# Optimization experiments

Measured on AMD Instinct MI355X. Metric: run time of the kernel, lower is better.

The kernel has to match this reference:

```python
import jax, jax.numpy as jnp
import numpy as np

L, B, S, D, N, H = 4, 4, 1024, 1024, 64, 16   # layers, batch, seq, d_model, d_state, heads
DI = 2 * D      # d_inner (expand_factor=2)
DH = D // H     # head dim
DF = 4 * D      # ffn hidden
SCALE = 1.0 / np.sqrt(DH)


def setup_inputs() -> dict:
    key = jax.random.key(0)
    ks = jax.random.split(key, 12)
    w = lambda k, sh: jax.random.normal(k, sh, jnp.float32) * 0.02
    return {
        "x": jax.random.normal(ks[0], (B, S, D), jnp.float32),
        "A_log": jax.random.normal(ks[1], (L, N), jnp.float32),
        "Dp": jax.random.normal(ks[2], (L, D), jnp.float32),
        "W_in": w(ks[3], (L, 2 * DI, D)), "b_in": jnp.zeros((L, 2 * DI), jnp.float32),
        "W_xp": w(ks[4], (L, N, DI)), "b_xp": jnp.zeros((L, N), jnp.float32),
        "W_dt": w(ks[5], (L, D, DI)), "b_dt": jnp.zeros((L, D), jnp.float32),
        "W_out": w(ks[6], (L, D, DI)), "b_out": jnp.zeros((L, D), jnp.float32),
        "W_qkv": w(ks[7], (L, 3 * D, D)), "b_qkv": jnp.zeros((L, 3 * D), jnp.float32),
        "W_ao": w(ks[8], (L, D, D)), "b_ao": jnp.zeros((L, D), jnp.float32),
        "g1": jnp.ones((L, D), jnp.float32), "be1": jnp.zeros((L, D), jnp.float32),
        "g2": jnp.ones((L, D), jnp.float32), "be2": jnp.zeros((L, D), jnp.float32),
        "W_f1": w(ks[9], (L, DF, D)), "b_f1": jnp.zeros((L, DF), jnp.float32),
        "W_f2": w(ks[10], (L, D, DF)), "b_f2": jnp.zeros((L, D), jnp.float32),
    }


def _ln(x, g, b, eps=1e-5):
    mu = x.mean(-1, keepdims=True)
    var = ((x - mu) ** 2).mean(-1, keepdims=True)
    return (x - mu) * jax.lax.rsqrt(var + eps) * g + b


def _mamba(x, A_log, Dp, W_in, b_in, W_xp, b_xp, W_dt, b_dt, W_out, b_out):
    xr = jnp.einsum('bsd,od->bso', x, W_in) + b_in          # [b,s,2*DI]
    xi, res = jnp.split(xr, 2, axis=-1)
    xi = jax.nn.silu(xi)
    A = -jnp.exp(A_log)                                      # [N]
    delta = jax.nn.softplus(jnp.einsum('bsi,di->bsd', xi, W_dt) + b_dt)  # [b,s,D]
    m = delta.mean(-1)                                       # [b,s]
    A_disc = jnp.exp(A[None, None, :] * m[:, :, None])       # [b,s,N]
    u = jnp.einsum('bsi,ni->bsn', xi, W_xp) + b_xp           # [b,s,N]

    def step(state, inp):
        a_t, u_t = inp
        state = a_t * state + u_t                            # [b,N]
        return state, state.sum(-1)                          # carry, emit sum over d_state

    init = jnp.zeros((x.shape[0], A_log.shape[0]), x.dtype)
    _, ssum = jax.lax.scan(step, init, (A_disc.swapaxes(0, 1), u.swapaxes(0, 1)))
    ssum = ssum.swapaxes(0, 1)                               # [b,s]
    y = ssum[..., None] * xi                                 # [b,s,DI]
    y = y * jax.nn.silu(res)
    y = jnp.einsum('bsi,di->bsd', y, W_out) + b_out
    return y + x * Dp


def _attn(x, W_qkv, b_qkv, W_ao, b_ao):
    b, s, d = x.shape
    qkv = jnp.einsum('bsd,od->bso', x, W_qkv) + b_qkv        # [b,s,3d]
    qkv = qkv.reshape(b, s, 3, H, DH)
    q = jnp.moveaxis(qkv[:, :, 0], 2, 1)                     # [b,h,s,dh]
    k = jnp.moveaxis(qkv[:, :, 1], 2, 1)
    v = jnp.moveaxis(qkv[:, :, 2], 2, 1)
    scores = jnp.einsum('bhqd,bhkd->bhqk', q, k) * SCALE
    wts = jax.nn.softmax(scores, axis=-1)
    o = jnp.einsum('bhqk,bhkd->bhqd', wts, v)
    o = jnp.moveaxis(o, 1, 2).reshape(b, s, d)
    return jnp.einsum('bsd,od->bso', o, W_ao) + b_ao


def _forward(x, A_log, Dp, W_in, b_in, W_xp, b_xp, W_dt, b_dt, W_out, b_out,
             W_qkv, b_qkv, W_ao, b_ao, g1, be1, g2, be2, W_f1, b_f1, W_f2, b_f2):
    for l in range(L):
        m = _mamba(x, A_log[l], Dp[l], W_in[l], b_in[l], W_xp[l], b_xp[l],
                   W_dt[l], b_dt[l], W_out[l], b_out[l])
        x = _ln(x + m, g1[l], be1[l])
        a = _attn(x, W_qkv[l], b_qkv[l], W_ao[l], b_ao[l])
        x = _ln(x + a, g2[l], be2[l])
        h = jax.nn.gelu(jnp.einsum('bsd,fd->bsf', x, W_f1[l]) + b_f1[l], approximate=False)
        x = x + jnp.einsum('bsf,df->bsd', h, W_f2[l]) + b_f2[l]
    return x


def reference(x, A_log, Dp, W_in, b_in, W_xp, b_xp, W_dt, b_dt, W_out, b_out,
              W_qkv, b_qkv, W_ao, b_ao, g1, be1, g2, be2, W_f1, b_f1, W_f2, b_f2):
    return _forward(x, A_log, Dp, W_in, b_in, W_xp, b_xp, W_dt, b_dt, W_out, b_out,
                    W_qkv, b_qkv, W_ao, b_ao, g1, be1, g2, be2, W_f1, b_f1, W_f2, b_f2)
```

## Files before the change

kernel.cpp:

```cpp
#include <hip/hip_runtime.h>
#include <math.h>

typedef unsigned short ushort_t;
typedef unsigned int uint_t;
typedef __attribute__((ext_vector_type(8))) short short8;
typedef __attribute__((ext_vector_type(4))) float f32x4;

constexpr int Bb = 4, Ss = 1024, Dd = 1024, Nn = 64, Hh = 16;
constexpr int DIi = 2048, DFf = 4096;
constexpr int TOKENS = Bb * Ss;

constexpr size_t O_IN  = 0;
constexpr size_t O_DT  = 4194304;
constexpr size_t O_XP  = O_DT + 2097152;
constexpr size_t O_OUT = O_XP + 262144;
constexpr size_t O_QKV = O_OUT + 2097152;
constexpr size_t O_AO  = O_QKV + 3145728;
constexpr size_t O_F1  = O_AO + 1048576;
constexpr size_t O_F2  = O_F1 + 4194304;
constexpr size_t W_TOTAL = O_F2 + 4194304;
constexpr size_t W_QUADS = W_TOTAL / 4;

enum { EPI_SPLIT = 0, EPI_QKV, EPI_GELU, EPI_DTXP, EPI_DP, EPI_F32, EPI_RESID };

__device__ __forceinline__ float siluf(float x) { return x / (1.f + expf(-x)); }
__device__ __forceinline__ float softplusf(float x) { return fmaxf(x, 0.f) + log1pf(expf(-fabsf(x))); }
__device__ __forceinline__ float geluf(float x) { return 0.5f * x * (1.f + erff(x * 0.7071067811865476f)); }

__device__ __forceinline__ float bf2f(uint_t u) {
    union { uint_t i; float f; } v; v.i = u << 16; return v.f;
}
__device__ __forceinline__ ushort_t f2bf(float f) {
    union { float f; uint_t i; } v; v.f = f;
    return (ushort_t)((v.i + 0x7FFFu + ((v.i >> 16) & 1u)) >> 16);
}

__device__ __forceinline__ void gload_lds16(const ushort_t* g, ushort_t* l) {
    __builtin_amdgcn_global_load_lds(
        (const __attribute__((address_space(1))) unsigned int*)g,
        (__attribute__((address_space(3))) unsigned int*)l, 16, 0, 0);
}

__device__ __forceinline__ void wait_vm(int n) {
    if (n == 0)      asm volatile("s_waitcnt vmcnt(0)" ::: "memory");
    else if (n == 3) asm volatile("s_waitcnt vmcnt(3)" ::: "memory");
    else if (n == 4) asm volatile("s_waitcnt vmcnt(4)" ::: "memory");
    else if (n == 6) asm volatile("s_waitcnt vmcnt(6)" ::: "memory");
    else             asm volatile("s_waitcnt vmcnt(8)" ::: "memory");
}

template <int EPI>
__global__ __launch_bounds__(512, 2) void gemm_wide256(
    const ushort_t* __restrict__ A, const ushort_t* __restrict__ Bw,
    const float* __restrict__ bias, int M, int N, int K,
    ushort_t* __restrict__ ob0, ushort_t* __restrict__ ob1)
{
    __shared__ __attribute__((aligned(16))) ushort_t AB[65536];
    const int tid = threadIdx.x;
    const int lane = tid & 63, wid = tid >> 6;
    const int wr = wid >> 2, wc = wid & 3;
    const int l15 = lane & 15, lg = lane >> 4;

    int bx = blockIdx.x, by = blockIdx.y;
    const int gx = gridDim.x, gy = gridDim.y;
    if ((gy & 3) == 0 && (gx & 1) == 0) {
        const int s = by * gx + bx;
        const int xcd = s & 7, c = s >> 3;
        const int gyc = gy >> 2, gxc = gx >> 1;
        by = (xcd & 3) * gyc + (c % gyc);
        bx = (xcd >> 2) * gxc + (c / gyc);
    }
    const int m0 = by << 8, n0 = bx << 8;

    f32x4 acc[8][4];
#pragma unroll
    for (int i = 0; i < 8; ++i)
#pragma unroll
        for (int j = 0; j < 4; ++j) { acc[i][j][0]=0.f; acc[i][j][1]=0.f; acc[i][j][2]=0.f; acc[i][j][3]=0.f; }

    const int srow8 = lane >> 3;
    const int scc8  = (lane & 7) ^ srow8;
    const ushort_t* Ag = A + (size_t)(m0 + wid * 32 + srow8) * K + scc8 * 8;
    const ushort_t* Bg = Bw + (size_t)(n0 + wid * 32 + srow8) * K + scc8 * 8;

    auto STAGE = [&](int b_, int k0_) {
        ushort_t* d_ = AB + b_ * 32768;
#pragma unroll
        for (int i = 0; i < 4; ++i) {
            gload_lds16(Ag + (size_t)i * 8 * K + k0_, d_ + (wid * 32 + i * 8) * 64);
            gload_lds16(Bg + (size_t)i * 8 * K + k0_, d_ + 16384 + (wid * 32 + i * 8) * 64);
        }
    };

    const int NS = K >> 6;
    STAGE(0, 0);
    wait_vm(0);
    __builtin_amdgcn_s_barrier();
    int cur = 0;
    for (int s = 0; s < NS; ++s) {
        if (s + 1 < NS) STAGE(cur ^ 1, (s + 1) << 6);
        const ushort_t* As_ = AB + cur * 32768;
        const ushort_t* Bs_ = As_ + 16384;
#pragma unroll
        for (int kk = 0; kk < 2; ++kk) {
            short8 af[8], bfr[4];
#pragma unroll
            for (int mi = 0; mi < 8; ++mi) {
                const int row = wr * 128 + mi * 16 + l15;
                const int ch = (kk * 4 + lg) ^ (row & 7);
                af[mi] = *(const short8*)&As_[row * 64 + ch * 8];
            }
#pragma unroll
            for (int nj = 0; nj < 4; ++nj) {
                const int row = wc * 64 + nj * 16 + l15;
                const int ch = (kk * 4 + lg) ^ (row & 7);
                bfr[nj] = *(const short8*)&Bs_[row * 64 + ch * 8];
            }
#pragma unroll
            for (int mi = 0; mi < 8; ++mi)
#pragma unroll
                for (int nj = 0; nj < 4; ++nj)
                    acc[mi][nj] = __builtin_amdgcn_mfma_f32_16x16x32_bf16(
                        af[mi], bfr[nj], acc[mi][nj], 0, 0, 0);
        }
        if (s + 1 < NS) {
            wait_vm(0);
            __builtin_amdgcn_s_barrier();
        }
        cur ^= 1;
    }
    __syncthreads();

    const bool lo = (EPI != EPI_SPLIT) || (n0 < DIi);
#pragma unroll
    for (int nj = 0; nj < 4; ++nj) {
        const int coll = wc * 64 + nj * 16 + l15;
        const float bv = bias[n0 + coll];
#pragma unroll
        for (int mi = 0; mi < 8; ++mi)
#pragma unroll
            for (int r = 0; r < 4; ++r) {
                float v = acc[mi][nj][r] + bv;
                if (EPI == EPI_SPLIT) v = lo ? siluf(v) : v;
                else v = geluf(v);
                AB[(wr * 128 + mi * 16 + lg * 4 + r) * 256 + coll] = f2bf(v);
            }
    }
    __syncthreads();
    ushort_t* dst = (EPI == EPI_SPLIT) ? (lo ? ob0 : ob1) : ob0;
    const int Nd = (EPI == EPI_SPLIT) ? DIi : N;
    const int nb = (EPI == EPI_SPLIT && !lo) ? (n0 - DIi) : n0;
#pragma unroll
    for (int it = 0; it < 16; ++it) {
        const int c = it * 512 + tid;
        const int row = c >> 5, ch = c & 31;
        *(uint4*)&dst[(size_t)(m0 + row) * Nd + nb + ch * 8] =
            *(const uint4*)&AB[row * 256 + ch * 8];
    }
}

template <int EPI, int MT, int NBUF, int XBY>
__global__ __launch_bounds__(256) void gemm_mfma(
    const ushort_t* __restrict__ A, const ushort_t* __restrict__ Bw,
    const float* __restrict__ bias, int M, int N, int K,
    float* __restrict__ of0, float* __restrict__ of1,
    ushort_t* __restrict__ ob0, ushort_t* __restrict__ ob1,
    const float* __restrict__ e0, const float* __restrict__ e1)
{
    constexpr int BUFSZ = (MT == 128) ? 8192 : 6144;
    constexpr int DEPTH = NBUF - 1;
    constexpr int L     = (MT == 128) ? 4 : 3;
    constexpr int NJ    = (MT == 128) ? 4 : 2;
    constexpr int XBX   = 8 / XBY;
    __shared__ __attribute__((aligned(16))) ushort_t AB[NBUF * BUFSZ];

    const int tid = threadIdx.x;
    const int lane = tid & 63, wid = tid >> 6;
    const int wr = (MT == 128) ? (wid >> 1) : 0;
    const int wc = (MT == 128) ? (wid & 1) : wid;
    const int l15 = lane & 15, lg = lane >> 4;

    int bx = blockIdx.x, by = blockIdx.y;
    const int gx = gridDim.x, gy = gridDim.y;
    if ((gy % XBY) == 0 && (gx % XBX) == 0) {
        const int s = by * gx + bx;
        const int xcd = s & 7, c = s >> 3;
        const int gyc = gy / XBY, gxc = gx / XBX;
        by = (xcd % XBY) * gyc + (c % gyc);
        bx = (xcd / XBY) * gxc + (c / gyc);
    }
    const int m0 = by * MT, n0 = bx << 7;

    f32x4 acc[4][NJ];
#pragma unroll
    for (int i = 0; i < 4; ++i)
#pragma unroll
        for (int j = 0; j < NJ; ++j) { acc[i][j][0] = 0.f; acc[i][j][1] = 0.f; acc[i][j][2] = 0.f; acc[i][j][3] = 0.f; }

    const int srow4 = lane >> 2;
    const int scc4  = (lane & 3) ^ ((lane >> 3) & 3);
    const ushort_t* Ag = A + (size_t)(m0 + wid * 32 + srow4) * K + scc4 * 8;
    const ushort_t* Bg = Bw + (size_t)(n0 + wid * 32 + srow4) * K + scc4 * 8;
    const ushort_t* sb64[3];
    int do64[3];
    if (MT == 64) {
#pragma unroll
        for (int j = 0; j < 3; ++j) {
            const int i = wid * 3 + j;
            const bool isA = i < 4;
            const int rb = (isA ? i : i - 4) * 16;
            sb64[j] = (isA ? A + (size_t)(m0 + rb + srow4) * K
                           : Bw + (size_t)(n0 + rb + srow4) * K) + scc4 * 8;
            do64[j] = (isA ? 0 : 2048) + rb * 32;
        }
    }

    auto STAGE = [&](int b_, int k0_) {
        ushort_t* d_ = AB + b_ * BUFSZ;
        if constexpr (MT == 128) {
            gload_lds16(Ag + k0_,                  d_ + (wid * 32) * 32);
            gload_lds16(Ag + (size_t)16 * K + k0_, d_ + (wid * 32 + 16) * 32);
            gload_lds16(Bg + k0_,                  d_ + 4096 + (wid * 32) * 32);
            gload_lds16(Bg + (size_t)16 * K + k0_, d_ + 4096 + (wid * 32 + 16) * 32);
        } else {
#pragma unroll
            for (int j = 0; j < 3; ++j)
                gload_lds16(sb64[j] + k0_, d_ + do64[j]);
        }
    };

    const int NS = K >> 5;
#pragma unroll
    for (int p = 0; p < DEPTH; ++p) STAGE(p, p * 32);
    wait_vm((DEPTH - 1) * L);
    __builtin_amdgcn_s_barrier();

    const int chAB = (lg ^ ((l15 >> 1) & 3)) * 8;
    int bc = 0, bp = DEPTH;
    for (int s = 0; s < NS; ++s) {
        if (s + DEPTH < NS) STAGE(bp, (s + DEPTH) << 5);
        const ushort_t* As_ = AB + bc * BUFSZ;
        const ushort_t* Bs_ = As_ + ((MT == 128) ? 4096 : 2048);
        short8 af[4], bfr[NJ];
#pragma unroll
        for (int mi = 0; mi < 4; ++mi)
            af[mi] = *(const short8*)&As_[(wr * 64 + mi * 16 + l15) * 32 + chAB];
#pragma unroll
        for (int nj = 0; nj < NJ; ++nj)
            bfr[nj] = *(const short8*)&Bs_[(wc * (MT == 128 ? 64 : 32) + nj * 16 + l15) * 32 + chAB];
#pragma unroll
        for (int mi = 0; mi < 4; ++mi)
#pragma unroll
            for (int nj = 0; nj < NJ; ++nj)
                acc[mi][nj] = __builtin_amdgcn_mfma_f32_16x16x32_bf16(
                    af[mi], bfr[nj], acc[mi][nj], 0, 0, 0);
        if (s + 1 < NS) {
            const int rem = NS - 2 - s;
            wait_vm(((rem < DEPTH - 1) ? rem : DEPTH - 1) * L);
            __builtin_amdgcn_s_barrier();
        }
        bc = (bc + 1 == NBUF) ? 0 : bc + 1;
        bp = (bp + 1 == NBUF) ? 0 : bp + 1;
    }
    __syncthreads();

    if constexpr (MT == 128) {
        const bool lo = (EPI != EPI_SPLIT) || (n0 < DIi);
#pragma unroll
        for (int nj = 0; nj < 4; ++nj) {
            const int coll = wc * 64 + nj * 16 + l15;
            const float bv = bias[n0 + coll];
#pragma unroll
            for (int mi = 0; mi < 4; ++mi)
#pragma unroll
                for (int r = 0; r < 4; ++r) {
                    float v = acc[mi][nj][r] + bv;
                    if (EPI == EPI_SPLIT) v = lo ? siluf(v) : v;
                    else if (EPI == EPI_GELU) v = geluf(v);
                    AB[(wr * 64 + mi * 16 + lg * 4 + r) * 128 + coll] = f2bf(v);
                }
        }
        __syncthreads();
        if (EPI == EPI_QKV && n0 >= 2048) {
            const int bb = m0 >> 10, srow0 = m0 & 1023;
#pragma unroll
            for (int it = 0; it < 8; ++it) {
                const int task = it * 256 + tid;
                const int dim = task & 127;
                const int strip = task >> 7;
                uint_t w[4];
#pragma unroll
                for (int j = 0; j < 4; ++j) {
                    const int s2 = strip * 8 + 2 * j;
                    w[j] = (uint_t)AB[s2 * 128 + dim] | ((uint_t)AB[(s2 + 1) * 128 + dim] << 16);
                }
                const int vd = (n0 - 2048) + dim;
                *(uint4*)&ob1[((size_t)(bb * Hh + (vd >> 6)) * 64 + (vd & 63)) * Ss + srow0 + strip * 8] =
                    make_uint4(w[0], w[1], w[2], w[3]);
            }
        } else {
            ushort_t* dst = (EPI == EPI_SPLIT) ? (lo ? ob0 : ob1) : ob0;
            const int Nd = (EPI == EPI_SPLIT) ? DIi : N;
            const int nb = (EPI == EPI_SPLIT && !lo) ? (n0 - DIi) : n0;
#pragma unroll
            for (int i = 0; i < 8; ++i) {
                const int c = i * 256 + tid;
                const int row = c >> 4, ch = c & 15;
                *(uint4*)&dst[(size_t)(m0 + row) * Nd + nb + ch * 8] =
                    *(const uint4*)&AB[row * 128 + ch * 8];
            }
        }
    } else {
        float* Cf = (float*)AB;
#pragma unroll
        for (int nj = 0; nj < NJ; ++nj) {
            const int coll = wc * 32 + nj * 16 + l15;
            const float bv = bias[n0 + coll];
#pragma unroll
            for (int mi = 0; mi < 4; ++mi)
#pragma unroll
                for (int r = 0; r < 4; ++r)
                    Cf[(mi * 16 + lg * 4 + r) * 128 + coll] = acc[mi][nj][r] + bv;
        }
        __syncthreads();
#pragma unroll
        for (int i = 0; i < 8; ++i) {
            const int c = i * 256 + tid;
            const int row = c >> 5, ch = c & 31;
            const int grow = m0 + row;
            const int gcol = n0 + ch * 4;
            float4 v = *(const float4*)&Cf[row * 128 + ch * 4];
            if (EPI == EPI_DTXP) {
                if (n0 < Dd) {
                    float ps = softplusf(v.x) + softplusf(v.y) + softplusf(v.z) + softplusf(v.w);
#pragma unroll
                    for (int off = 1; off < 32; off <<= 1) ps += __shfl_xor(ps, off);
                    if ((lane & 31) == 0)
                        of0[(size_t)grow * 8 + (n0 >> 7)] = ps;
                } else {
                    *(float4*)&of1[(size_t)grow * 128 + (gcol - Dd)] = v;
                }
            } else if (EPI == EPI_DP) {
                const float4 e = *(const float4*)&e0[(size_t)grow * N + gcol];
                const float4 d = *(const float4*)&e1[gcol];
                v.x = fmaf(e.x, d.x, v.x); v.y = fmaf(e.y, d.y, v.y);
                v.z = fmaf(e.z, d.z, v.z); v.w = fmaf(e.w, d.w, v.w);
                *(float4*)&of0[(size_t)grow * N + gcol] = v;
            } else if (EPI == EPI_F32) {
                *(float4*)&of0[(size_t)grow * N + gcol] = v;
            } else {
                const float4 e = *(const float4*)&e0[(size_t)grow * N + gcol];
                v.x += e.x; v.y += e.y; v.z += e.z; v.w += e.w;
                *(float4*)&of0[(size_t)grow * N + gcol] = v;
                uint2 w;
                w.x = (uint_t)f2bf(v.x) | ((uint_t)f2bf(v.y) << 16);
                w.y = (uint_t)f2bf(v.z) | ((uint_t)f2bf(v.w) << 16);
                *(uint2*)&ob0[(size_t)grow * N + gcol] = w;
            }
        }
    }
}

__global__ __launch_bounds__(256) void convert_weights_kernel(
    const float* __restrict__ Win, const float* __restrict__ Wdt,
    const float* __restrict__ Wxp, const float* __restrict__ Wout,
    const float* __restrict__ Wqkv, const float* __restrict__ Wao,
    const float* __restrict__ Wf1, const float* __restrict__ Wf2,
    const float* __restrict__ bdt, const float* __restrict__ bxp,
    ushort_t* __restrict__ dst, float* __restrict__ bcat)
{
    size_t q = (size_t)blockIdx.x * blockDim.x + threadIdx.x;
    if (q < 288) {
#pragma unroll
        for (int j = 0; j < 4; ++j) {
            const int e = (int)q * 4 + j;
            bcat[e] = (e < Dd) ? bdt[e] : ((e < Dd + Nn) ? bxp[e - Dd] : 0.f);
        }
    }
    const size_t stride = (size_t)gridDim.x * blockDim.x;
    for (; q < W_QUADS; q += stride) {
        const size_t e = q * 4;
        float4 v;
        if (e < O_DT)       v = *(const float4*)&Win[e - O_IN];
        else if (e < O_XP)  v = *(const float4*)&Wdt[e - O_DT];
        else if (e < O_OUT) {
            const size_t li = e - O_XP;
            const int row = (int)(li >> 11), colq = (int)(li & 2047);
            v = (row < Nn) ? *(const float4*)&Wxp[(size_t)row * DIi + colq]
                           : make_float4(0.f, 0.f, 0.f, 0.f);
        }
        else if (e < O_QKV) v = *(const float4*)&Wout[e - O_OUT];
        else if (e < O_AO)  v = *(const float4*)&Wqkv[e - O_QKV];
        else if (e < O_F1)  v = *(const float4*)&Wao[e - O_AO];
        else if (e < O_F2)  v = *(const float4*)&Wf1[e - O_F1];
        else                v = *(const float4*)&Wf2[e - O_F2];
        uint2 w;
        w.x = (uint_t)f2bf(v.x) | ((uint_t)f2bf(v.y) << 16);
        w.y = (uint_t)f2bf(v.z) | ((uint_t)f2bf(v.w) << 16);
        *(uint2*)&dst[e] = w;
    }
}

__global__ __launch_bounds__(256) void cvt_f32_bf16_kernel(
    const float* __restrict__ in, ushort_t* __restrict__ out)
{
    const size_t i4 = (size_t)blockIdx.x * blockDim.x + threadIdx.x;
    const float4 v = *(const float4*)&in[i4 * 4];
    uint2 w;
    w.x = (uint_t)f2bf(v.x) | ((uint_t)f2bf(v.y) << 16);
    w.y = (uint_t)f2bf(v.z) | ((uint_t)f2bf(v.w) << 16);
    *(uint2*)&out[i4 * 4] = w;
}

__global__ __launch_bounds__(256) void ln_residual_kernel(
    float* __restrict__ xio, const float* __restrict__ addin,
    const float* __restrict__ g, const float* __restrict__ be,
    ushort_t* __restrict__ xb)
{
    __shared__ float red[8];
    const int tid = threadIdx.x;
    const size_t base = (size_t)blockIdx.x * Dd;
    const float4 xv = *(const float4*)&xio[base + tid * 4];
    const float4 av = *(const float4*)&addin[base + tid * 4];
    float v[4] = {xv.x + av.x, xv.y + av.y, xv.z + av.z, xv.w + av.w};
    float s = v[0] + v[1] + v[2] + v[3];
    float s2 = v[0] * v[0] + v[1] * v[1] + v[2] * v[2] + v[3] * v[3];
#pragma unroll
    for (int off = 32; off; off >>= 1) { s += __shfl_xor(s, off); s2 += __shfl_xor(s2, off); }
    if ((tid & 63) == 0) { red[tid >> 6] = s; red[4 + (tid >> 6)] = s2; }
    __syncthreads();
    const float mu = (red[0] + red[1] + red[2] + red[3]) * (1.f / (float)Dd);
    const float var = (red[4] + red[5] + red[6] + red[7]) * (1.f / (float)Dd) - mu * mu;
    const float rstd = rsqrtf(var + 1e-5f);
    const float4 gv = *(const float4*)&g[tid * 4];
    const float4 bv = *(const float4*)&be[tid * 4];
    float o[4];
    o[0] = (v[0] - mu) * rstd * gv.x + bv.x;
    o[1] = (v[1] - mu) * rstd * gv.y + bv.y;
    o[2] = (v[2] - mu) * rstd * gv.z + bv.z;
    o[3] = (v[3] - mu) * rstd * gv.w + bv.w;
    *(float4*)&xio[base + tid * 4] = make_float4(o[0], o[1], o[2], o[3]);
    uint2 w;
    w.x = (uint_t)f2bf(o[0]) | ((uint_t)f2bf(o[1]) << 16);
    w.y = (uint_t)f2bf(o[2]) | ((uint_t)f2bf(o[3]) << 16);
    *(uint2*)&xb[base + tid * 4] = w;
}

__global__ __launch_bounds__(1024) void scan_fused_kernel(
    const float* __restrict__ A_log_l, const float* __restrict__ part,
    const float* __restrict__ u, float* __restrict__ ssum)
{
    __shared__ float Ps[16][64];
    __shared__ float Sl[16][64];
    __shared__ float Cs[16][64];
    __shared__ float Ms[16][64];
    const int b = blockIdx.x;
    const int tid = threadIdx.x;
    const int n = tid & 63, c = tid >> 6;
    const int t0 = b * Ss + c * 64;
    const float Aval = -expf(A_log_l[n]);

    {
        const float* pp = part + (size_t)(t0 + n) * 8;
        float ps = 0.f;
#pragma unroll
        for (int j = 0; j < 8; ++j) ps += pp[j];
        Ms[c][n] = ps * (1.f / 1024.f);
    }
    __syncthreads();

    float S = 0.f, msum = 0.f;
#pragma unroll 8
    for (int t = 0; t < 64; ++t) {
        const float mt = Ms[c][t];
        msum += mt;
        S = fmaf(expf(Aval * mt), S, u[(size_t)(t0 + t) * 128 + n]);
    }
    Ps[c][n] = expf(Aval * msum);
    Sl[c][n] = S;
    __syncthreads();

    if (c == 0) {
        float carry = 0.f;
#pragma unroll
        for (int cc = 0; cc < 16; ++cc) {
            Cs[cc][n] = carry;
            carry = fmaf(Ps[cc][n], carry, Sl[cc][n]);
        }
    }
    __syncthreads();

    float st = Cs[c][n];
#pragma unroll 4
    for (int t = 0; t < 64; ++t) {
        st = fmaf(expf(Aval * Ms[c][t]), st, u[(size_t)(t0 + t) * 128 + n]);
        float r = st;
#pragma unroll
        for (int off = 32; off; off >>= 1) r += __shfl_xor(r, off);
        if (n == 0) ssum[t0 + t] = r;
    }
}

__global__ __launch_bounds__(256) void y_gate_kernel(
    ushort_t* __restrict__ xi, const ushort_t* __restrict__ res,
    const float* __restrict__ ssum)
{
    const size_t i8 = (size_t)blockIdx.x * blockDim.x + threadIdx.x;
    const int t = (int)(i8 >> 8);
    const float sv = ssum[t];
    uint4 xw = *(const uint4*)&xi[i8 * 8];
    const uint4 rw = *(const uint4*)&res[i8 * 8];
    const uint_t xs[4] = {xw.x, xw.y, xw.z, xw.w};
    const uint_t rs[4] = {rw.x, rw.y, rw.z, rw.w};
    uint_t os[4];
#pragma unroll
    for (int j = 0; j < 4; ++j) {
        const float x0 = bf2f(xs[j] & 0xffffu), x1 = bf2f(xs[j] >> 16);
        const float r0 = bf2f(rs[j] & 0xffffu), r1 = bf2f(rs[j] >> 16);
        os[j] = (uint_t)f2bf(sv * x0 * siluf(r0)) | ((uint_t)f2bf(sv * x1 * siluf(r1)) << 16);
    }
    *(uint4*)&xi[i8 * 8] = make_uint4(os[0], os[1], os[2], os[3]);
}

__global__ __launch_bounds__(256) void attn_mfma_kernel(
    const ushort_t* __restrict__ qkv, const ushort_t* __restrict__ vt,
    ushort_t* __restrict__ out)
{
    __shared__ ushort_t Ks[2][64 * 64];
    __shared__ ushort_t Vs[2][64 * 64];
    __shared__ __attribute__((aligned(16))) ushort_t Pb[4][2560];

    const int tid = threadIdx.x;
    const int lane = tid & 63, wid = tid >> 6;
    const int b = blockIdx.z, h = blockIdx.y;
    const int q0 = blockIdx.x * 128 + wid * 32;
    const int l15 = lane & 15, lg = lane >> 4;
    constexpr float CEXP = 0.125f * 1.44269504f;

    short8 qf[2][2];
#pragma unroll
    for (int mi = 0; mi < 2; ++mi)
#pragma unroll
        for (int kk = 0; kk < 2; ++kk)
            qf[mi][kk] = *(const short8*)&qkv[(size_t)(b * Ss + q0 + mi * 16 + l15) * 3072
                                              + h * 64 + kk * 32 + lg * 8];

    f32x4 oacc[2][4];
#pragma unroll
    for (int mi = 0; mi < 2; ++mi)
#pragma unroll
        for (int nj = 0; nj < 4; ++nj) { oacc[mi][nj][0]=0.f; oacc[mi][nj][1]=0.f; oacc[mi][nj][2]=0.f; oacc[mi][nj][3]=0.f; }
    float lrun[2][4];
#pragma unroll
    for (int mi = 0; mi < 2; ++mi)
#pragma unroll
        for (int r = 0; r < 4; ++r) lrun[mi][r] = 0.f;

    const int srow = lane >> 3;
    const int scc  = (lane & 7) ^ srow;
    const ushort_t* Kg = qkv + (size_t)(b * Ss + wid * 16 + srow) * 3072 + 1024 + h * 64 + scc * 8;
    const ushort_t* Vg = vt + (size_t)((b * Hh + h) * 64 + wid * 16 + srow) * Ss + scc * 8;

    auto STAGE_KV = [&](int buf, int kt) {
#pragma unroll
        for (int j = 0; j < 2; ++j) {
            gload_lds16(Kg + (size_t)(kt * 64 + j * 8) * 3072, Ks[buf] + (wid * 16 + j * 8) * 64);
            gload_lds16(Vg + (size_t)j * 8 * Ss + kt * 64,     Vs[buf] + (wid * 16 + j * 8) * 64);
        }
    };

    constexpr int NT = Ss / 64;
    STAGE_KV(0, 0);
    int cur = 0;
    for (int kt = 0; kt < NT; ++kt) {
        if (kt + 1 < NT) STAGE_KV(cur ^ 1, kt + 1);
        wait_vm((kt + 1 < NT) ? 4 : 0);
        __builtin_amdgcn_s_barrier();

        f32x4 sacc[2][4];
#pragma unroll
        for (int mi = 0; mi < 2; ++mi)
#pragma unroll
            for (int nj = 0; nj < 4; ++nj) { sacc[mi][nj][0]=0.f; sacc[mi][nj][1]=0.f; sacc[mi][nj][2]=0.f; sacc[mi][nj][3]=0.f; }
        __builtin_amdgcn_s_setprio(1);
#pragma unroll
        for (int kk = 0; kk < 2; ++kk) {
            short8 kf[4];
#pragma unroll
            for (int nj = 0; nj < 4; ++nj) {
                const int row = nj * 16 + l15;
                const int ch = (kk * 4 + lg) ^ (row & 7);
                kf[nj] = *(const short8*)&Ks[cur][row * 64 + ch * 8];
            }
#pragma unroll
            for (int mi = 0; mi < 2; ++mi)
#pragma unroll
                for (int nj = 0; nj < 4; ++nj)
                    sacc[mi][nj] = __builtin_amdgcn_mfma_f32_16x16x32_bf16(
                        qf[mi][kk], kf[nj], sacc[mi][nj], 0, 0, 0);
        }
        __builtin_amdgcn_s_setprio(0);

#pragma unroll
        for (int mi = 0; mi < 2; ++mi)
#pragma unroll
            for (int nj = 0; nj < 4; ++nj) {
                const int bi = mi * 2 + (nj >> 1);
                const int chsw = ((nj & 1) * 2 + (l15 >> 3)) ^ lg;
#pragma unroll
                for (int r = 0; r < 4; ++r) {
                    const float p = exp2f(sacc[mi][nj][r] * CEXP);
                    lrun[mi][r] += p;
                    const int q15 = lg * 4 + r;
                    Pb[wid][bi * 640 + q15 * 40 + chsw * 8 + (lane & 7)] = f2bf(p);
                }
            }

        __builtin_amdgcn_s_setprio(1);
#pragma unroll
        for (int kk = 0; kk < 2; ++kk) {
            short8 pa[2], vb[4];
#pragma unroll
            for (int mi = 0; mi < 2; ++mi) {
                const int chsw = lg ^ (l15 >> 2);
                pa[mi] = *(const short8*)&Pb[wid][(mi * 2 + kk) * 640 + l15 * 40 + chsw * 8];
            }
#pragma unroll
            for (int nj = 0; nj < 4; ++nj) {
                const int row = nj * 16 + l15;
                const int ch = (kk * 4 + lg) ^ (row & 7);
                vb[nj] = *(const short8*)&Vs[cur][row * 64 + ch * 8];
            }
#pragma unroll
            for (int mi = 0; mi < 2; ++mi)
#pragma unroll
                for (int nj = 0; nj < 4; ++nj)
                    oacc[mi][nj] = __builtin_amdgcn_mfma_f32_16x16x32_bf16(
                        pa[mi], vb[nj], oacc[mi][nj], 0, 0, 0);
        }
        __builtin_amdgcn_s_setprio(0);

        asm volatile("s_waitcnt lgkmcnt(0)" ::: "memory");
        __builtin_amdgcn_s_barrier();
        cur ^= 1;
    }

#pragma unroll
    for (int mi = 0; mi < 2; ++mi)
#pragma unroll
        for (int r = 0; r < 4; ++r) {
            float s = lrun[mi][r];
#pragma unroll
            for (int off = 1; off < 16; off <<= 1) s += __shfl_xor(s, off);
            lrun[mi][r] = 1.f / s;
        }
#pragma unroll
    for (int mi = 0; mi < 2; ++mi)
#pragma unroll
        for (int r = 0; r < 4; ++r) {
            const int q = q0 + mi * 16 + lg * 4 + r;
            const float inv = lrun[mi][r];
#pragma unroll
            for (int nj = 0; nj < 4; ++nj)
                out[(size_t)(b * Ss + q) * Dd + h * 64 + nj * 16 + l15] =
                    f2bf(oacc[mi][nj][r] * inv);
        }
}

extern "C" void kernel_launch(void* const* d_in, const int* in_sizes, int n_in,
                              void* d_out, int out_size, void* d_ws, size_t ws_size,
                              hipStream_t stream)
{
    const float* x_in  = (const float*)d_in[0];
    const float* A_log = (const float*)d_in[1];
    const float* Dp    = (const float*)d_in[2];
    const float* W_in  = (const float*)d_in[3];
    const float* b_in  = (const float*)d_in[4];
    const float* W_xp  = (const float*)d_in[5];
    const float* b_xp  = (const float*)d_in[6];
    const float* W_dt  = (const float*)d_in[7];
    const float* b_dt  = (const float*)d_in[8];
    const float* W_out = (const float*)d_in[9];
    const float* b_out = (const float*)d_in[10];
    const float* W_qkv = (const float*)d_in[11];
    const float* b_qkv = (const float*)d_in[12];
    const float* W_ao  = (const float*)d_in[13];
    const float* b_ao  = (const float*)d_in[14];
    const float* g1    = (const float*)d_in[15];
    const float* be1   = (const float*)d_in[16];
    const float* g2    = (const float*)d_in[17];
    const float* be2   = (const float*)d_in[18];
    const float* W_f1  = (const float*)d_in[19];
    const float* b_f1  = (const float*)d_in[20];
    const float* W_f2  = (const float*)d_in[21];
    const float* b_f2  = (const float*)d_in[22];

    float* xf      = (float*)d_ws;
    float* a3      = xf + 4194304;
    float* ub      = a3 + 4194304;
    float* sb      = ub + 524288;
    float* part    = sb + 4096;
    float* bcat    = part + 32768;
    ushort_t* xb    = (ushort_t*)(bcat + 1152);
    ushort_t* xi_b  = xb + 4194304;
    ushort_t* res_b = xi_b + 8388608;
    ushort_t* qh_b  = res_b + 8388608;
    ushort_t* ao_b  = qh_b + 16777216;
    ushort_t* Wb    = ao_b + 4194304;
    ushort_t* vt_b  = Wb + W_TOTAL;

    hipMemcpyAsync(xf, x_in, (size_t)TOKENS * Dd * sizeof(float),
                   hipMemcpyDeviceToDevice, stream);
    cvt_f32_bf16_kernel<<<dim3(4096), dim3(256), 0, stream>>>(x_in, xb);

    const dim3 blk(256), blk512(512);

    for (int l = 0; l < 4; ++l) {
        convert_weights_kernel<<<dim3(2048), blk, 0, stream>>>(
            W_in + (size_t)l * 4194304, W_dt + (size_t)l * 2097152,
            W_xp + (size_t)l * 131072,  W_out + (size_t)l * 2097152,
            W_qkv + (size_t)l * 3145728, W_ao + (size_t)l * 1048576,
            W_f1 + (size_t)l * 4194304, W_f2 + (size_t)l * 4194304,
            b_dt + (size_t)l * 1024, b_xp + (size_t)l * Nn, Wb, bcat);

        gemm_wide256<EPI_SPLIT><<<dim3(16, 16), blk512, 0, stream>>>(
            xb, Wb + O_IN, b_in + (size_t)l * 4096, TOKENS, 4096, 1024,
            xi_b, res_b);
        gemm_mfma<EPI_DTXP, 64, 4, 8><<<dim3(9, 64), blk, 0, stream>>>(
            xi_b, Wb + O_DT, bcat, TOKENS, 1152, 2048,
            part, ub, nullptr, nullptr, nullptr, nullptr);
        scan_fused_kernel<<<dim3(Bb), dim3(1024), 0, stream>>>(
            A_log + (size_t)l * Nn, part, ub, sb);
        y_gate_kernel<<<dim3(4096), blk, 0, stream>>>(xi_b, res_b, sb);
        gemm_mfma<EPI_DP, 64, 4, 8><<<dim3(8, 64), blk, 0, stream>>>(
            xi_b, Wb + O_OUT, b_out + (size_t)l * 1024, TOKENS, 1024, 2048,
            a3, nullptr, nullptr, nullptr, xf, Dp + (size_t)l * 1024);
        ln_residual_kernel<<<dim3(TOKENS), blk, 0, stream>>>(
            xf, a3, g1 + (size_t)l * 1024, be1 + (size_t)l * 1024, xb);
        gemm_mfma<EPI_QKV, 128, 3, 4><<<dim3(24, 32), blk, 0, stream>>>(
            xb, Wb + O_QKV, b_qkv + (size_t)l * 3072, TOKENS, 3072, 1024,
            nullptr, nullptr, qh_b, vt_b, nullptr, nullptr);
        attn_mfma_kernel<<<dim3(8, Hh, Bb), blk, 0, stream>>>(qh_b, vt_b, ao_b);
        gemm_mfma<EPI_F32, 64, 4, 8><<<dim3(8, 64), blk, 0, stream>>>(
            ao_b, Wb + O_AO, b_ao + (size_t)l * 1024, TOKENS, 1024, 1024,
            a3, nullptr, nullptr, nullptr, nullptr, nullptr);
        ln_residual_kernel<<<dim3(TOKENS), blk, 0, stream>>>(
            xf, a3, g2 + (size_t)l * 1024, be2 + (size_t)l * 1024, xb);
        gemm_wide256<EPI_GELU><<<dim3(16, 16), blk512, 0, stream>>>(
            xb, Wb + O_F1, b_f1 + (size_t)l * 4096, TOKENS, 4096, 1024,
            qh_b, nullptr);
        gemm_mfma<EPI_RESID, 64, 4, 8><<<dim3(8, 64), blk, 0, stream>>>(
            qh_b, Wb + O_F2, b_f2 + (size_t)l * 1024, TOKENS, 1024, 4096,
            xf, nullptr, xb, nullptr, xf, nullptr);
    }

    hipMemcpyAsync(d_out, xf, (size_t)TOKENS * Dd * sizeof(float),
                   hipMemcpyDeviceToDevice, stream);
    (void)in_sizes; (void)n_in; (void)out_size; (void)ws_size;
}
```

Baseline: 1.723 ms.

## Split 64-row GEMMs into a K=64 double-buffered kernel with XOR-swizzled LDS

Moves the 64-row-tile GEMM path out of the templated gemm_mfma into a new gemm_narrow64 kernel. It stages K=64 slices per step with two buffers instead of K=32 slices with a 4-deep ring, and uses an 8-way XOR swizzle across 64-wide rows. The aim is to halve the number of barriers and waits per K and to give the MFMAs more work per step. In exchange the pipeline is only one stage deep with a full vmcnt(0) wait each step, so less memory latency may be hidden. The 128-tile path is only simplified, with no behaviour change.

```diff
diff --git a/kernel.cpp b/kernel.cpp
--- a/kernel.cpp
+++ b/kernel.cpp
@@ -43,10 +43,9 @@
 
 __device__ __forceinline__ void wait_vm(int n) {
     if (n == 0)      asm volatile("s_waitcnt vmcnt(0)" ::: "memory");
-    else if (n == 3) asm volatile("s_waitcnt vmcnt(3)" ::: "memory");
     else if (n == 4) asm volatile("s_waitcnt vmcnt(4)" ::: "memory");
-    else if (n == 6) asm volatile("s_waitcnt vmcnt(6)" ::: "memory");
-    else             asm volatile("s_waitcnt vmcnt(8)" ::: "memory");
+    else if (n == 8) asm volatile("s_waitcnt vmcnt(8)" ::: "memory");
+    else             asm volatile("s_waitcnt vmcnt(0)" ::: "memory");
 }
 
 template <int EPI>
@@ -159,26 +158,22 @@
     }
 }
 
-template <int EPI, int MT, int NBUF, int XBY>
-__global__ __launch_bounds__(256) void gemm_mfma(
+template <int EPI, int XBY>
+__global__ __launch_bounds__(256) void gemm_narrow64(
     const ushort_t* __restrict__ A, const ushort_t* __restrict__ Bw,
     const float* __restrict__ bias, int M, int N, int K,
     float* __restrict__ of0, float* __restrict__ of1,
-    ushort_t* __restrict__ ob0, ushort_t* __restrict__ ob1,
+    ushort_t* __restrict__ ob0,
     const float* __restrict__ e0, const float* __restrict__ e1)
 {
-    constexpr int BUFSZ = (MT == 128) ? 8192 : 6144;
-    constexpr int DEPTH = NBUF - 1;
-    constexpr int L     = (MT == 128) ? 4 : 3;
-    constexpr int NJ    = (MT == 128) ? 4 : 2;
-    constexpr int XBX   = 8 / XBY;
-    __shared__ __attribute__((aligned(16))) ushort_t AB[NBUF * BUFSZ];
+    constexpr int BUFSZ = 12288;
+    __shared__ __attribute__((aligned(16))) ushort_t AB[2 * BUFSZ];
 
     const int tid = threadIdx.x;
     const int lane = tid & 63, wid = tid >> 6;
-    const int wr = (MT == 128) ? (wid >> 1) : 0;
-    const int wc = (MT == 128) ? (wid & 1) : wid;
+    const int wc = wid;
     const int l15 = lane & 15, lg = lane >> 4;
+    constexpr int XBX = 8 / XBY;
 
     int bx = blockIdx.x, by = blockIdx.y;
     const int gx = gridDim.x, gy = gridDim.y;
@@ -189,44 +184,168 @@
         by = (xcd % XBY) * gyc + (c % gyc);
         bx = (xcd / XBY) * gxc + (c / gyc);
     }
-    const int m0 = by * MT, n0 = bx << 7;
-
-    f32x4 acc[4][NJ];
+    const int m0 = by * 64, n0 = bx << 7;
+
+    f32x4 acc[4][2];
 #pragma unroll
     for (int i = 0; i < 4; ++i)
 #pragma unroll
-        for (int j = 0; j < NJ; ++j) { acc[i][j][0] = 0.f; acc[i][j][1] = 0.f; acc[i][j][2] = 0.f; acc[i][j][3] = 0.f; }
+        for (int j = 0; j < 2; ++j) { acc[i][j][0]=0.f; acc[i][j][1]=0.f; acc[i][j][2]=0.f; acc[i][j][3]=0.f; }
+
+    const int srow8 = lane >> 3;
+    const int scc8  = (lane & 7) ^ srow8;
+    const ushort_t* sb[6];
+    int dofs[6];
+#pragma unroll
+    for (int j = 0; j < 6; ++j) {
+        const int i = wid * 6 + j;
+        const bool isA = i < 8;
+        const int rb = (isA ? i : i - 8) * 8;
+        sb[j] = (isA ? A + (size_t)(m0 + rb + srow8) * K
+                     : Bw + (size_t)(n0 + rb + srow8) * K) + scc8 * 8;
+        dofs[j] = (isA ? 0 : 4096) + rb * 64;
+    }
+
+    auto STAGE = [&](int b_, int k0_) {
+        ushort_t* d_ = AB + b_ * BUFSZ;
+#pragma unroll
+        for (int j = 0; j < 6; ++j)
+            gload_lds16(sb[j] + k0_, d_ + dofs[j]);
+    };
+
+    const int NS = K >> 6;
+    STAGE(0, 0);
+    wait_vm(0);
+    __builtin_amdgcn_s_barrier();
+    int cur = 0;
+    for (int s = 0; s < NS; ++s) {
+        if (s + 1 < NS) STAGE(cur ^ 1, (s + 1) << 6);
+        const ushort_t* As_ = AB + cur * BUFSZ;
+        const ushort_t* Bs_ = As_ + 4096;
+#pragma unroll
+        for (int kk = 0; kk < 2; ++kk) {
+            short8 af[4], bfr[2];
+#pragma unroll
+            for (int mi = 0; mi < 4; ++mi) {
+                const int row = mi * 16 + l15;
+                const int ch = (kk * 4 + lg) ^ (row & 7);
+                af[mi] = *(const short8*)&As_[row * 64 + ch * 8];
+            }
+#pragma unroll
+            for (int nj = 0; nj < 2; ++nj) {
+                const int row = wc * 32 + nj * 16 + l15;
+                const int ch = (kk * 4 + lg) ^ (row & 7);
+                bfr[nj] = *(const short8*)&Bs_[row * 64 + ch * 8];
+            }
+#pragma unroll
+            for (int mi = 0; mi < 4; ++mi)
+#pragma unroll
+                for (int nj = 0; nj < 2; ++nj)
+                    acc[mi][nj] = __builtin_amdgcn_mfma_f32_16x16x32_bf16(
+                        af[mi], bfr[nj], acc[mi][nj], 0, 0, 0);
+        }
+        if (s + 1 < NS) {
+            wait_vm(0);
+            __builtin_amdgcn_s_barrier();
+        }
+        cur ^= 1;
+    }
+    __syncthreads();
+
+    float* Cf = (float*)AB;
+#pragma unroll
+    for (int nj = 0; nj < 2; ++nj) {
+        const int coll = wc * 32 + nj * 16 + l15;
+        const float bv = bias[n0 + coll];
+#pragma unroll
+        for (int mi = 0; mi < 4; ++mi)
+#pragma unroll
+            for (int r = 0; r < 4; ++r)
+                Cf[(mi * 16 + lg * 4 + r) * 128 + coll] = acc[mi][nj][r] + bv;
+    }
+    __syncthreads();
+#pragma unroll
+    for (int i = 0; i < 8; ++i) {
+        const int c = i * 256 + tid;
+        const int row = c >> 5, ch = c & 31;
+        const int grow = m0 + row;
+        const int gcol = n0 + ch * 4;
+        float4 v = *(const float4*)&Cf[row * 128 + ch * 4];
+        if (EPI == EPI_DTXP) {
+            if (n0 < Dd) {
+                float ps = softplusf(v.x) + softplusf(v.y) + softplusf(v.z) + softplusf(v.w);
+#pragma unroll
+                for (int off = 1; off < 32; off <<= 1) ps += __shfl_xor(ps, off);
+                if ((lane & 31) == 0)
+                    of0[(size_t)grow * 8 + (n0 >> 7)] = ps;
+            } else {
+                *(float4*)&of1[(size_t)grow * 128 + (gcol - Dd)] = v;
+            }
+        } else if (EPI == EPI_DP) {
+            const float4 e = *(const float4*)&e0[(size_t)grow * N + gcol];
+            const float4 d = *(const float4*)&e1[gcol];
+            v.x = fmaf(e.x, d.x, v.x); v.y = fmaf(e.y, d.y, v.y);
+            v.z = fmaf(e.z, d.z, v.z); v.w = fmaf(e.w, d.w, v.w);
+            *(float4*)&of0[(size_t)grow * N + gcol] = v;
+        } else if (EPI == EPI_F32) {
+            *(float4*)&of0[(size_t)grow * N + gcol] = v;
+        } else {
+            const float4 e = *(const float4*)&e0[(size_t)grow * N + gcol];
+            v.x += e.x; v.y += e.y; v.z += e.z; v.w += e.w;
+            *(float4*)&of0[(size_t)grow * N + gcol] = v;
+            uint2 w;
+            w.x = (uint_t)f2bf(v.x) | ((uint_t)f2bf(v.y) << 16);
+            w.y = (uint_t)f2bf(v.z) | ((uint_t)f2bf(v.w) << 16);
+            *(uint2*)&ob0[(size_t)grow * N + gcol] = w;
+        }
+    }
+}
+
+template <int EPI, int NBUF, int XBY>
+__global__ __launch_bounds__(256) void gemm_mfma(
+    const ushort_t* __restrict__ A, const ushort_t* __restrict__ Bw,
+    const float* __restrict__ bias, int M, int N, int K,
+    ushort_t* __restrict__ ob0, ushort_t* __restrict__ ob1)
+{
+    constexpr int BUFSZ = 8192;
+    constexpr int DEPTH = NBUF - 1;
+    constexpr int L     = 4;
+    constexpr int XBX   = 8 / XBY;
+    __shared__ __attribute__((aligned(16))) ushort_t AB[NBUF * BUFSZ];
+
+    const int tid = threadIdx.x;
+    const int lane = tid & 63, wid = tid >> 6;
+    const int wr = wid >> 1, wc = wid & 1;
+    const int l15 = lane & 15, lg = lane >> 4;
+
+    int bx = blockIdx.x, by = blockIdx.y;
+    const int gx = gridDim.x, gy = gridDim.y;
+    if ((gy % XBY) == 0 && (gx % XBX) == 0) {
+        const int s = by * gx + bx;
+        const int xcd = s & 7, c = s >> 3;
+        const int gyc = gy / XBY, gxc = gx / XBX;
+        by = (xcd % XBY) * gyc + (c % gyc);
+        bx = (xcd / XBY) * gxc + (c / gyc);
+    }
+    const int m0 = by * 128, n0 = bx << 7;
+
+    f32x4 acc[4][4];
+#pragma unroll
+    for (int i = 0; i < 4; ++i)
+#pragma unroll
+        for (int j = 0; j < 4; ++j) { acc[i][j][0] = 0.f; acc[i][j][1] = 0.f; acc[i][j][2] = 0.f; acc[i][j][3] = 0.f; }
 
     const int srow4 = lane >> 2;
     const int scc4  = (lane & 3) ^ ((lane >> 3) & 3);
     const ushort_t* Ag = A + (size_t)(m0 + wid * 32 + srow4) * K + scc4 * 8;
     const ushort_t* Bg = Bw + (size_t)(n0 + wid * 32 + srow4) * K + scc4 * 8;
-    const ushort_t* sb64[3];
-    int do64[3];
-    if (MT == 64) {
-#pragma unroll
-        for (int j = 0; j < 3; ++j) {
-            const int i = wid * 3 + j;
-            const bool isA = i < 4;
-            const int rb = (isA ? i : i - 4) * 16;
-            sb64[j] = (isA ? A + (size_t)(m0 + rb + srow4) * K
-                           : Bw + (size_t)(n0 + rb + srow4) * K) + scc4 * 8;
-            do64[j] = (isA ? 0 : 2048) + rb * 32;
-        }
-    }
 
     auto STAGE = [&](int b_, int k0_) {
         ushort_t* d_ = AB + b_ * BUFSZ;
-        if constexpr (MT == 128) {
-            gload_lds16(Ag + k0_,                  d_ + (wid * 32) * 32);
-            gload_lds16(Ag + (size_t)16 * K + k0_, d_ + (wid * 32 + 16) * 32);
-            gload_lds16(Bg + k0_,                  d_ + 4096 + (wid * 32) * 32);
-            gload_lds16(Bg + (size_t)16 * K + k0_, d_ + 4096 + (wid * 32 + 16) * 32);
-        } else {
-#pragma unroll
-            for (int j = 0; j < 3; ++j)
-                gload_lds16(sb64[j] + k0_, d_ + do64[j]);
-        }
+        gload_lds16(Ag + k0_,                  d_ + (wid * 32) * 32);
+        gload_lds16(Ag + (size_t)16 * K + k0_, d_ + (wid * 32 + 16) * 32);
+        gload_lds16(Bg + k0_,                  d_ + 4096 + (wid * 32) * 32);
+        gload_lds16(Bg + (size_t)16 * K + k0_, d_ + 4096 + (wid * 32 + 16) * 32);
     };
 
     const int NS = K >> 5;
@@ -240,18 +359,18 @@
     for (int s = 0; s < NS; ++s) {
         if (s + DEPTH < NS) STAGE(bp, (s + DEPTH) << 5);
         const ushort_t* As_ = AB + bc * BUFSZ;
-        const ushort_t* Bs_ = As_ + ((MT == 128) ? 4096 : 2048);
-        short8 af[4], bfr[NJ];
+        const ushort_t* Bs_ = As_ + 4096;
+        short8 af[4], bfr[4];
 #pragma unroll
         for (int mi = 0; mi < 4; ++mi)
             af[mi] = *(const short8*)&As_[(wr * 64 + mi * 16 + l15) * 32 + chAB];
 #pragma unroll
-        for (int nj = 0; nj < NJ; ++nj)
-            bfr[nj] = *(const short8*)&Bs_[(wc * (MT == 128 ? 64 : 32) + nj * 16 + l15) * 32 + chAB];
+        for (int nj = 0; nj < 4; ++nj)
+            bfr[nj] = *(const short8*)&Bs_[(wc * 64 + nj * 16 + l15) * 32 + chAB];
 #pragma unroll
         for (int mi = 0; mi < 4; ++mi)
 #pragma unroll
-            for (int nj = 0; nj < NJ; ++nj)
+            for (int nj = 0; nj < 4; ++nj)
                 acc[mi][nj] = __builtin_amdgcn_mfma_f32_16x16x32_bf16(
                     af[mi], bfr[nj], acc[mi][nj], 0, 0, 0);
         if (s + 1 < NS) {
@@ -264,99 +383,41 @@
     }
     __syncthreads();
 
-    if constexpr (MT == 128) {
-        const bool lo = (EPI != EPI_SPLIT) || (n0 < DIi);
-#pragma unroll
-        for (int nj = 0; nj < 4; ++nj) {
-            const int coll = wc * 64 + nj * 16 + l15;
-            const float bv = bias[n0 + coll];
-#pragma unroll
-            for (int mi = 0; mi < 4; ++mi)
-#pragma unroll
-                for (int r = 0; r < 4; ++r) {
-                    float v = acc[mi][nj][r] + bv;
-                    if (EPI == EPI_SPLIT) v = lo ? siluf(v) : v;
-                    else if (EPI == EPI_GELU) v = geluf(v);
-                    AB[(wr * 64 + mi * 16 + lg * 4 + r) * 128 + coll] = f2bf(v);
-                }
-        }
-        __syncthreads();
-        if (EPI == EPI_QKV && n0 >= 2048) {
-            const int bb = m0 >> 10, srow0 = m0 & 1023;
-#pragma unroll
-            for (int it = 0; it < 8; ++it) {
-                const int task = it * 256 + tid;
-                const int dim = task & 127;
-                const int strip = task >> 7;
-                uint_t w[4];
-#pragma unroll
-                for (int j = 0; j < 4; ++j) {
-                    const int s2 = strip * 8 + 2 * j;
-                    w[j] = (uint_t)AB[s2 * 128 + dim] | ((uint_t)AB[(s2 + 1) * 128 + dim] << 16);
-                }
-                const int vd = (n0 - 2048) + dim;
-                *(uint4*)&ob1[((size_t)(bb * Hh + (vd >> 6)) * 64 + (vd & 63)) * Ss + srow0 + strip * 8] =
-                    make_uint4(w[0], w[1], w[2], w[3]);
-            }
-        } else {
-            ushort_t* dst = (EPI == EPI_SPLIT) ? (lo ? ob0 : ob1) : ob0;
-            const int Nd = (EPI == EPI_SPLIT) ? DIi : N;
-            const int nb = (EPI == EPI_SPLIT && !lo) ? (n0 - DIi) : n0;
-#pragma unroll
-            for (int i = 0; i < 8; ++i) {
-                const int c = i * 256 + tid;
-                const int row = c >> 4, ch = c & 15;
-                *(uint4*)&dst[(size_t)(m0 + row) * Nd + nb + ch * 8] =
-                    *(const uint4*)&AB[row * 128 + ch * 8];
-            }
+#pragma unroll
+    for (int nj = 0; nj < 4; ++nj) {
+        const int coll = wc * 64 + nj * 16 + l15;
+        const float bv = bias[n0 + coll];
+#pragma unroll
+        for (int mi = 0; mi < 4; ++mi)
+#pragma unroll
+            for (int r = 0; r < 4; ++r)
+                AB[(wr * 64 + mi * 16 + lg * 4 + r) * 128 + coll] = f2bf(acc[mi][nj][r] + bv);
+    }
+    __syncthreads();
+    if (EPI == EPI_QKV && n0 >= 2048) {
+        const int bb = m0 >> 10, srow0 = m0 & 1023;
+#pragma unroll
+        for (int it = 0; it < 8; ++it) {
+            const int task = it * 256 + tid;
+            const int dim = task & 127;
+            const int strip = task >> 7;
+            uint_t w[4];
+#pragma unroll
+            for (int j = 0; j < 4; ++j) {
+                const int s2 = strip * 8 + 2 * j;
+                w[j] = (uint_t)AB[s2 * 128 + dim] | ((uint_t)AB[(s2 + 1) * 128 + dim] << 16);
+            }
+            const int vd = (n0 - 2048) + dim;
+            *(uint4*)&ob1[((size_t)(bb * Hh + (vd >> 6)) * 64 + (vd & 63)) * Ss + srow0 + strip * 8] =
+                make_uint4(w[0], w[1], w[2], w[3]);
         }
     } else {
-        float* Cf = (float*)AB;
-#pragma unroll
-        for (int nj = 0; nj < NJ; ++nj) {
-            const int coll = wc * 32 + nj * 16 + l15;
-            const float bv = bias[n0 + coll];
-#pragma unroll
-            for (int mi = 0; mi < 4; ++mi)
-#pragma unroll
-                for (int r = 0; r < 4; ++r)
-                    Cf[(mi * 16 + lg * 4 + r) * 128 + coll] = acc[mi][nj][r] + bv;
-        }
-        __syncthreads();
 #pragma unroll
         for (int i = 0; i < 8; ++i) {
             const int c = i * 256 + tid;
-            const int row = c >> 5, ch = c & 31;
-            const int grow = m0 + row;
-            const int gcol = n0 + ch * 4;
-            float4 v = *(const float4*)&Cf[row * 128 + ch * 4];
-            if (EPI == EPI_DTXP) {
-                if (n0 < Dd) {
-                    float ps = softplusf(v.x) + softplusf(v.y) + softplusf(v.z) + softplusf(v.w);
-#pragma unroll
-                    for (int off = 1; off < 32; off <<= 1) ps += __shfl_xor(ps, off);
-                    if ((lane & 31) == 0)
-                        of0[(size_t)grow * 8 + (n0 >> 7)] = ps;
-                } else {
-                    *(float4*)&of1[(size_t)grow * 128 + (gcol - Dd)] = v;
-                }
-            } else if (EPI == EPI_DP) {
-                const float4 e = *(const float4*)&e0[(size_t)grow * N + gcol];
-                const float4 d = *(const float4*)&e1[gcol];
-                v.x = fmaf(e.x, d.x, v.x); v.y = fmaf(e.y, d.y, v.y);
-                v.z = fmaf(e.z, d.z, v.z); v.w = fmaf(e.w, d.w, v.w);
-                *(float4*)&of0[(size_t)grow * N + gcol] = v;
-            } else if (EPI == EPI_F32) {
-                *(float4*)&of0[(size_t)grow * N + gcol] = v;
-            } else {
-                const float4 e = *(const float4*)&e0[(size_t)grow * N + gcol];
-                v.x += e.x; v.y += e.y; v.z += e.z; v.w += e.w;
-                *(float4*)&of0[(size_t)grow * N + gcol] = v;
-                uint2 w;
-                w.x = (uint_t)f2bf(v.x) | ((uint_t)f2bf(v.y) << 16);
-                w.y = (uint_t)f2bf(v.z) | ((uint_t)f2bf(v.w) << 16);
-                *(uint2*)&ob0[(size_t)grow * N + gcol] = w;
-            }
+            const int row = c >> 4, ch = c & 15;
+            *(uint4*)&ob0[(size_t)(m0 + row) * N + n0 + ch * 8] =
+                *(const uint4*)&AB[row * 128 + ch * 8];
         }
     }
 }
@@ -726,32 +787,32 @@
         gemm_wide256<EPI_SPLIT><<<dim3(16, 16), blk512, 0, stream>>>(
             xb, Wb + O_IN, b_in + (size_t)l * 4096, TOKENS, 4096, 1024,
             xi_b, res_b);
-        gemm_mfma<EPI_DTXP, 64, 4, 8><<<dim3(9, 64), blk, 0, stream>>>(
+        gemm_narrow64<EPI_DTXP, 8><<<dim3(9, 64), blk, 0, stream>>>(
             xi_b, Wb + O_DT, bcat, TOKENS, 1152, 2048,
-            part, ub, nullptr, nullptr, nullptr, nullptr);
+            part, ub, nullptr, nullptr, nullptr);
         scan_fused_kernel<<<dim3(Bb), dim3(1024), 0, stream>>>(
             A_log + (size_t)l * Nn, part, ub, sb);
         y_gate_kernel<<<dim3(4096), blk, 0, stream>>>(xi_b, res_b, sb);
-        gemm_mfma<EPI_DP, 64, 4, 8><<<dim3(8, 64), blk, 0, stream>>>(
+        gemm_narrow64<EPI_DP, 8><<<dim3(8, 64), blk, 0, stream>>>(
             xi_b, Wb + O_OUT, b_out + (size_t)l * 1024, TOKENS, 1024, 2048,
-            a3, nullptr, nullptr, nullptr, xf, Dp + (size_t)l * 1024);
+            a3, nullptr, nullptr, xf, Dp + (size_t)l * 1024);
         ln_residual_kernel<<<dim3(TOKENS), blk, 0, stream>>>(
             xf, a3, g1 + (size_t)l * 1024, be1 + (size_t)l * 1024, xb);
-        gemm_mfma<EPI_QKV, 128, 3, 4><<<dim3(24, 32), blk, 0, stream>>>(
+        gemm_mfma<EPI_QKV, 3, 4><<<dim3(24, 32), blk, 0, stream>>>(
             xb, Wb + O_QKV, b_qkv + (size_t)l * 3072, TOKENS, 3072, 1024,
-            nullptr, nullptr, qh_b, vt_b, nullptr, nullptr);
+            qh_b, vt_b);
         attn_mfma_kernel<<<dim3(8, Hh, Bb), blk, 0, stream>>>(qh_b, vt_b, ao_b);
-        gemm_mfma<EPI_F32, 64, 4, 8><<<dim3(8, 64), blk, 0, stream>>>(
+        gemm_narrow64<EPI_F32, 8><<<dim3(8, 64), blk, 0, stream>>>(
             ao_b, Wb + O_AO, b_ao + (size_t)l * 1024, TOKENS, 1024, 1024,
-            a3, nullptr, nullptr, nullptr, nullptr, nullptr);
+            a3, nullptr, nullptr, nullptr, nullptr);
         ln_residual_kernel<<<dim3(TOKENS), blk, 0, stream>>>(
             xf, a3, g2 + (size_t)l * 1024, be2 + (size_t)l * 1024, xb);
         gemm_wide256<EPI_GELU><<<dim3(16, 16), blk512, 0, stream>>>(
             xb, Wb + O_F1, b_f1 + (size_t)l * 4096, TOKENS, 4096, 1024,
             qh_b, nullptr);
-        gemm_mfma<EPI_RESID, 64, 4, 8><<<dim3(8, 64), blk, 0, stream>>>(
+        gemm_narrow64<EPI_RESID, 8><<<dim3(8, 64), blk, 0, stream>>>(
             qh_b, Wb + O_F2, b_f2 + (size_t)l * 1024, TOKENS, 1024, 4096,
-            xf, nullptr, xb, nullptr, xf, nullptr);
+            xf, nullptr, xb, xf, nullptr);
     }
 
     hipMemcpyAsync(d_out, xf, (size_t)TOKENS * Dd * sizeof(float),
```

New measurement: 1.629 ms, median of 2. 1.06x faster.
